# Kernel optimization log

Measured on AMD Instinct MI355X. Metric: run time of the kernel, lower is better.

## Reference

```python
import jax, jax.numpy as jnp
import numpy as np

GROUPS = 8          # 4-bit groups per row (one scale/offset each)
VALS_PER_GROUP = 8  # nibbles packed per int32 weight word
MID = GROUPS * VALS_PER_GROUP  # fixed inner dim = 64


def _unpack4(x, n):
    """Unpack n little-endian 4-bit nibbles from int32 array x -> [..., n]."""
    shifts = (jnp.arange(n, dtype=jnp.int32) * 4)
    return jnp.right_shift(x[..., None], shifts) & 15


def setup_inputs() -> dict:
    key = jax.random.key(0)
    k1, k2, k3, k4 = jax.random.split(key, 4)
    N0, N1 = 8192, 8192
    scale = jax.random.normal(k1, (N0, GROUPS), dtype=jnp.float32)
    offset = jax.random.randint(k2, (N0,), 0, 2147483647, dtype=jnp.int32)
    weight = jax.random.randint(k3, (N0, GROUPS), 0, 2147483647, dtype=jnp.int32)
    activation = jax.random.normal(k4, (MID, N1), dtype=jnp.float32)
    return {"scale": scale, "offset": offset, "weight": weight, "activation": activation}


def reference(scale, offset, weight, activation):
    # weight: [N0, 8] int32, each word packs 8 nibbles -> [N0, 8, 8] -> MID=64
    w = _unpack4(weight, VALS_PER_GROUP).astype(jnp.float32)   # [N0, G, V]
    # offset: [N0] int32 packs one 4-bit offset per group -> [N0, G]
    off = _unpack4(offset, GROUPS).astype(jnp.float32)         # [N0, G]
    # per-group dequant: scale * (w - offset)
    dq = scale[:, :, None] * (w - off[:, :, None])             # [N0, G, V]
    dq = dq.reshape(scale.shape[0], MID)                       # [N0, 64]
    return dq @ activation                                     # [N0, N1]
```

## Files before the change

### kernel.cpp

```cpp
#include <hip/hip_runtime.h>
#include <hip/hip_bf16.h>

#define M_DIM 8192
#define N_DIM 8192

typedef short short8 __attribute__((ext_vector_type(8)));
typedef float f32x4 __attribute__((ext_vector_type(4)));

static __device__ __forceinline__ short f2bf(float f) {
    __hip_bfloat16 h = __float2bfloat16(f);
    union { __hip_bfloat16 h; short s; } u;
    u.h = h;
    return u.s;
}

__global__ __launch_bounds__(256, 2) void gemm_dq(const float* __restrict__ scale,
                                                  const int* __restrict__ offset,
                                                  const int* __restrict__ weight,
                                                  const float* __restrict__ act,
                                                  float* __restrict__ C) {
    __shared__ float cs[4][64 * 32];

    const int tid  = threadIdx.x;
    const int lane = tid & 63;
    const int wid  = tid >> 6;
    const int l15  = lane & 15;
    const int l4   = lane >> 4;

    const int bn = (int)blockIdx.x & 63;
    const int mg = (int)blockIdx.x >> 6;
    const int n0   = bn * 128 + (wid & 1) * 64;
    const int wrow = (wid >> 1) * 64;

    short8 bfrag[2][4];
    #pragma unroll
    for (int kh = 0; kh < 2; ++kh) {
        #pragma unroll
        for (int fn = 0; fn < 4; ++fn) {
            const float* ap = act + (size_t)(kh * 32 + l4 * 8) * N_DIM + (n0 + fn * 16 + l15);
            short8 b;
            #pragma unroll
            for (int j = 0; j < 8; ++j) {
                b[j] = f2bf(ap[(size_t)j * N_DIM]);
            }
            bfrag[kh][fn] = b;
        }
    }

    float* ws = &cs[wid][0];
    const int rot = ((mg >> 2) & 1) * 4;

    #pragma unroll 2
    for (int ti = 0; ti < 8; ++ti) {
        const int t  = (ti + rot) & 7;
        const int m0 = (mg * 8 + t) * 128 + wrow;

        short8 afrag[2][4];
        #pragma unroll
        for (int kh = 0; kh < 2; ++kh) {
            const int g = kh * 4 + l4;
            #pragma unroll
            for (int fm = 0; fm < 4; ++fm) {
                const int m = m0 + fm * 16 + l15;
                const unsigned w = (unsigned)weight[m * 8 + g];
                const float   s = scale[m * 8 + g];
                const int   off = (int)(((unsigned)offset[m] >> (4 * g)) & 15u);
                short8 a;
                #pragma unroll
                for (int j = 0; j < 8; ++j) {
                    const int wv = (int)((w >> (4 * j)) & 15u);
                    a[j] = f2bf(s * (float)(wv - off));
                }
                afrag[kh][fm] = a;
            }
        }

        #pragma unroll
        for (int pass = 0; pass < 2; ++pass) {
            f32x4 acc[4][2] = {};
            #pragma unroll
            for (int fm = 0; fm < 4; ++fm) {
                #pragma unroll
                for (int fl = 0; fl < 2; ++fl) {
                    acc[fm][fl] = __builtin_amdgcn_mfma_f32_16x16x32_bf16(
                        afrag[0][fm], bfrag[0][pass * 2 + fl], acc[fm][fl], 0, 0, 0);
                    acc[fm][fl] = __builtin_amdgcn_mfma_f32_16x16x32_bf16(
                        afrag[1][fm], bfrag[1][pass * 2 + fl], acc[fm][fl], 0, 0, 0);
                }
            }

            #pragma unroll
            for (int fm = 0; fm < 4; ++fm) {
                #pragma unroll
                for (int fl = 0; fl < 2; ++fl) {
                    const int col = fl * 16 + l15;
                    #pragma unroll
                    for (int j = 0; j < 4; ++j) {
                        const int row = fm * 16 + l4 * 4 + j;
                        const int swz = ((((col >> 2) ^ (row & 7)) << 2) | (col & 3));
                        ws[row * 32 + swz] = acc[fm][fl][j];
                    }
                }
            }
            asm volatile("s_waitcnt lgkmcnt(0)" ::: "memory");

            #pragma unroll
            for (int r = 0; r < 8; ++r) {
                const int row = r * 8 + (lane >> 3);
                const int cb  = lane & 7;
                const f32x4 v = *reinterpret_cast<const f32x4*>(
                    &ws[row * 32 + ((cb ^ (row & 7)) << 2)]);
                const size_t gr = (size_t)(m0 + row);
                const size_t gc = (size_t)(n0 + pass * 32 + cb * 4);
                __builtin_nontemporal_store(v, reinterpret_cast<f32x4*>(&C[gr * N_DIM + gc]));
            }
        }
    }
}

extern "C" void kernel_launch(void* const* d_in, const int* in_sizes, int n_in,
                              void* d_out, int out_size, void* d_ws, size_t ws_size,
                              hipStream_t stream) {
    const float* scale  = (const float*)d_in[0];
    const int*   offset = (const int*)d_in[1];
    const int*   weight = (const int*)d_in[2];
    const float* act    = (const float*)d_in[3];
    float* out  = (float*)d_out;

    gemm_dq<<<512, 256, 0, stream>>>(scale, offset, weight, act, out);
}
```

Before: 58.98 us.

## Give each wave full 128-column strips and stage 16x128 output tiles

Each wave now owns 32 rows by all 128 block columns instead of a 64x64 quadrant, so it holds 8 B fragments (more registers) and dequantizes fewer A rows per tile. The epilogue writes 16-row by 128-column tiles through padded shared memory (stride 132) rather than an XOR swizzle. Each store instruction then covers two full 512-byte row segments, which should make global writes more contiguous. The trade-off is higher VGPR pressure from the larger bfrag array, plus possible LDS bank conflicts from the new padding.

```diff
diff --git a/kernel.cpp b/kernel.cpp
--- a/kernel.cpp
+++ b/kernel.cpp
@@ -19,7 +19,7 @@
                                                   const int* __restrict__ weight,
                                                   const float* __restrict__ act,
                                                   float* __restrict__ C) {
-    __shared__ float cs[4][64 * 32];
+    __shared__ float cs[4][16 * 132];
 
     const int tid  = threadIdx.x;
     const int lane = tid & 63;
@@ -29,14 +29,13 @@
 
     const int bn = (int)blockIdx.x & 63;
     const int mg = (int)blockIdx.x >> 6;
-    const int n0   = bn * 128 + (wid & 1) * 64;
-    const int wrow = (wid >> 1) * 64;
+    const int n0 = bn * 128;
 
-    short8 bfrag[2][4];
+    short8 bfrag[2][8];
     #pragma unroll
     for (int kh = 0; kh < 2; ++kh) {
         #pragma unroll
-        for (int fn = 0; fn < 4; ++fn) {
+        for (int fn = 0; fn < 8; ++fn) {
             const float* ap = act + (size_t)(kh * 32 + l4 * 8) * N_DIM + (n0 + fn * 16 + l15);
             short8 b;
             #pragma unroll
@@ -53,14 +52,14 @@
     #pragma unroll 2
     for (int ti = 0; ti < 8; ++ti) {
         const int t  = (ti + rot) & 7;
-        const int m0 = (mg * 8 + t) * 128 + wrow;
+        const int m0 = (mg * 8 + t) * 128 + wid * 32;
 
-        short8 afrag[2][4];
         #pragma unroll
-        for (int kh = 0; kh < 2; ++kh) {
-            const int g = kh * 4 + l4;
+        for (int fm = 0; fm < 2; ++fm) {
+            short8 afrag[2];
             #pragma unroll
-            for (int fm = 0; fm < 4; ++fm) {
+            for (int kh = 0; kh < 2; ++kh) {
+                const int g = kh * 4 + l4;
                 const int m = m0 + fm * 16 + l15;
                 const unsigned w = (unsigned)weight[m * 8 + g];
                 const float   s = scale[m * 8 + g];
@@ -71,48 +70,37 @@
                     const int wv = (int)((w >> (4 * j)) & 15u);
                     a[j] = f2bf(s * (float)(wv - off));
                 }
-                afrag[kh][fm] = a;
+                afrag[kh] = a;
             }
-        }
 
-        #pragma unroll
-        for (int pass = 0; pass < 2; ++pass) {
-            f32x4 acc[4][2] = {};
+            f32x4 acc[8] = {};
             #pragma unroll
-            for (int fm = 0; fm < 4; ++fm) {
-                #pragma unroll
-                for (int fl = 0; fl < 2; ++fl) {
-                    acc[fm][fl] = __builtin_amdgcn_mfma_f32_16x16x32_bf16(
-                        afrag[0][fm], bfrag[0][pass * 2 + fl], acc[fm][fl], 0, 0, 0);
-                    acc[fm][fl] = __builtin_amdgcn_mfma_f32_16x16x32_bf16(
-                        afrag[1][fm], bfrag[1][pass * 2 + fl], acc[fm][fl], 0, 0, 0);
-                }
+            for (int fn = 0; fn < 8; ++fn) {
+                acc[fn] = __builtin_amdgcn_mfma_f32_16x16x32_bf16(
+                    afrag[0], bfrag[0][fn], acc[fn], 0, 0, 0);
+                acc[fn] = __builtin_amdgcn_mfma_f32_16x16x32_bf16(
+                    afrag[1], bfrag[1][fn], acc[fn], 0, 0, 0);
             }
 
             #pragma unroll
-            for (int fm = 0; fm < 4; ++fm) {
+            for (int fn = 0; fn < 8; ++fn) {
+                const int col = fn * 16 + l15;
                 #pragma unroll
-                for (int fl = 0; fl < 2; ++fl) {
-                    const int col = fl * 16 + l15;
-                    #pragma unroll
-                    for (int j = 0; j < 4; ++j) {
-                        const int row = fm * 16 + l4 * 4 + j;
-                        const int swz = ((((col >> 2) ^ (row & 7)) << 2) | (col & 3));
-                        ws[row * 32 + swz] = acc[fm][fl][j];
-                    }
+                for (int j = 0; j < 4; ++j) {
+                    const int row16 = l4 * 4 + j;
+                    ws[row16 * 132 + col] = acc[fn][j];
                 }
             }
             asm volatile("s_waitcnt lgkmcnt(0)" ::: "memory");
 
             #pragma unroll
-            for (int r = 0; r < 8; ++r) {
-                const int row = r * 8 + (lane >> 3);
-                const int cb  = lane & 7;
-                const f32x4 v = *reinterpret_cast<const f32x4*>(
-                    &ws[row * 32 + ((cb ^ (row & 7)) << 2)]);
-                const size_t gr = (size_t)(m0 + row);
-                const size_t gc = (size_t)(n0 + pass * 32 + cb * 4);
-                __builtin_nontemporal_store(v, reinterpret_cast<f32x4*>(&C[gr * N_DIM + gc]));
+            for (int s = 0; s < 8; ++s) {
+                const int row16 = s * 2 + (lane >> 5);
+                const int c4    = (lane & 31) * 4;
+                const f32x4 v = *reinterpret_cast<const f32x4*>(&ws[row16 * 132 + c4]);
+                const size_t gr = (size_t)(m0 + fm * 16 + row16);
+                __builtin_nontemporal_store(v, reinterpret_cast<f32x4*>(
+                    &C[gr * N_DIM + n0 + c4]));
             }
         }
     }
```

Measured after the change: 51.15 us. -13.3%, faster.
